# Optimization experiments

Hardware: AMD Instinct MI355X
Metric: run time of the kernel (lower is better)

Reference implementation:

```python
import jax, jax.numpy as jnp
import numpy as np


def setup_inputs() -> dict:
    key = jax.random.key(0)
    k1, k2 = jax.random.split(key)
    M, F, V = 4, 4, 6
    # positive messages / factor values (probabilities in real MPA), keep denominators safe
    IVF = jax.random.uniform(k1, (M, F, V), dtype=jnp.float32) + 0.1
    fa_n = jax.random.uniform(k2, (F, M, M, M), dtype=jnp.float32) + 0.1
    # canonical 4x6 SCMA factor graph: FN f connects to 3 VNs; each VN to 2 FNs
    FN_index = jnp.array([[0, 1, 2], [0, 3, 4], [1, 3, 5], [2, 4, 5]], dtype=jnp.int32)
    VN_index = jnp.array([[0, 0, 0, 1, 1, 2], [1, 2, 3, 2, 3, 3]], dtype=jnp.int32)
    w0 = jnp.ones((M, F, V), dtype=jnp.float32)  # nn.Parameter(torch.ones([4,4,6]))
    return {"num_M": 4, "num_FN": 4, "num_VN": 6, "IVF": IVF, "VN_index": VN_index,
            "m": 0, "n": 1, "FN_index": FN_index, "fa_n": fa_n, "w0": w0}


def _mpa_forward(IVF, fa_n, w0, FN_index, VN_index, num_M, num_FN, num_VN, m, n):
    M, F, V = num_M, num_FN, num_VN
    fidx = jnp.arange(F)
    # gather: g[k][mm, f] = IVF[mm, f, FN_index[f, k]]
    g0 = IVF[:, fidx, FN_index[:, 0]]  # [M, F]
    g1 = IVF[:, fidx, FN_index[:, 1]]
    g2 = IVF[:, fidx, FN_index[:, 2]]
    # FN -> VN messages: sum over the two other users' symbols (m2=b, m3=c)
    A0 = jnp.einsum('bf,cf,fcab->af', g1, g2, fa_n)  # to FN_index[:,0]
    A1 = jnp.einsum('bf,cf,fcba->af', g0, g2, fa_n)  # to FN_index[:,1]
    A2 = jnp.einsum('bf,cf,fabc->af', g0, g1, fa_n)  # to FN_index[:,2]
    IFV = jnp.zeros((M, F, V), IVF.dtype)
    IFV = IFV.at[:, fidx, FN_index[:, 0]].add(A0)
    IFV = IFV.at[:, fidx, FN_index[:, 1]].add(A1)
    IFV = IFV.at[:, fidx, FN_index[:, 2]].add(A2)
    if m >= n:  # static python ints -> plain branch, matches `if m < n`
        return IVF
    IVF_sum = IFV.mean(axis=0)  # [F, V]; == sum_i (1/M) IFV[i]
    vidx = jnp.arange(V)
    va, vb = VN_index[0], VN_index[1]  # the two FNs each VN connects to
    new_a = (1.0 / M) * IFV[:, vb, vidx] / IVF_sum[vb, vidx]  # [M, V]
    new_b = (1.0 / M) * IFV[:, va, vidx] / IVF_sum[va, vidx]
    IVF = IVF.at[:, va, vidx].set(new_a)
    IVF = IVF.at[:, vb, vidx].set(new_b)
    return IVF * w0


def reference(num_M, num_FN, num_VN, IVF, VN_index, m, n, FN_index, fa_n, w0):
    return _mpa_forward(IVF, fa_n, w0, FN_index, VN_index, num_M, num_FN, num_VN, m, n)
```

## Files before the change

### kernel.cpp

```cpp
#include <hip/hip_runtime.h>

__global__ __launch_bounds__(128) void mpa_kernel(
    const float* __restrict__ IVF,
    const int*   __restrict__ VN,
    const int*   __restrict__ mPtr,
    const int*   __restrict__ nPtr,
    const int*   __restrict__ FN,
    const float* __restrict__ fa,
    const float* __restrict__ w0,
    float*       __restrict__ out)
{
    __shared__ float sIVF[96];
    __shared__ float sIFV[96];
    __shared__ float sSum[24];

    const int t = threadIdx.x;

    if (t < 96) {
        sIVF[t] = IVF[t];
        sIFV[t] = 0.0f;
    }
    __syncthreads();

    if (t < 48) {
        const int kind = t >> 4;
        const int r    = t & 15;
        const int a    = r >> 2;
        const int f    = r & 3;
        const int j0 = FN[f * 3 + 0];
        const int j1 = FN[f * 3 + 1];
        const int j2 = FN[f * 3 + 2];

        const int jb = (kind == 0) ? j1 : j0;
        const int jc = (kind == 2) ? j1 : j2;

        float gb[4], gc[4];
        #pragma unroll
        for (int i = 0; i < 4; ++i) {
            gb[i] = sIVF[i * 24 + f * 6 + jb];
            gc[i] = sIVF[i * 24 + f * 6 + jc];
        }

        float acc = 0.0f;
        #pragma unroll
        for (int c = 0; c < 4; ++c) {
            #pragma unroll
            for (int b = 0; b < 4; ++b) {
                int faIdx;
                if (kind == 0)      faIdx = f * 64 + c * 16 + a * 4 + b;
                else if (kind == 1) faIdx = f * 64 + c * 16 + b * 4 + a;
                else                faIdx = f * 64 + a * 16 + b * 4 + c;
                acc += gb[b] * gc[c] * fa[faIdx];
            }
        }

        const int jout = (kind == 0) ? j0 : ((kind == 1) ? j1 : j2);
        sIFV[a * 24 + f * 6 + jout] = acc;
    }
    __syncthreads();

    if (t < 24) {
        sSum[t] = 0.25f * (sIFV[0 * 24 + t] + sIFV[1 * 24 + t] +
                           sIFV[2 * 24 + t] + sIFV[3 * 24 + t]);
    }
    __syncthreads();

    if (t < 96) {
        const int mv = mPtr[0];
        const int nv = nPtr[0];
        if (mv >= nv) {
            out[t] = sIVF == nullptr ? 0.0f : sIVF[t] * 0.0f + IVF[t];
        } else {
            const int a   = t / 24;
            const int rem = t - a * 24;
            const int f   = rem / 6;
            const int v   = rem - f * 6;
            const int va  = VN[v];
            const int vb  = VN[6 + v];
            float val;
            if (f == va)      val = 0.25f * sIFV[a * 24 + vb * 6 + v] / sSum[vb * 6 + v];
            else if (f == vb) val = 0.25f * sIFV[a * 24 + va * 6 + v] / sSum[va * 6 + v];
            else              val = sIVF[t];
            out[t] = val * w0[t];
        }
    }
}

extern "C" void kernel_launch(void* const* d_in, const int* in_sizes, int n_in,
                              void* d_out, int out_size, void* d_ws, size_t ws_size,
                              hipStream_t stream) {
    (void)in_sizes; (void)n_in; (void)d_ws; (void)ws_size; (void)out_size;
    const float* IVF = (const float*)d_in[3];
    const int*   VN  = (const int*)  d_in[4];
    const int*   m   = (const int*)  d_in[5];
    const int*   n   = (const int*)  d_in[6];
    const int*   FN  = (const int*)  d_in[7];
    const float* fa  = (const float*)d_in[8];
    const float* w0  = (const float*)d_in[9];
    float*       out = (float*)d_out;

    mpa_kernel<<<1, 128, 0, stream>>>(IVF, VN, m, n, FN, fa, w0, out);
}
```

Before: 9.621 us.

## Collapse MPA kernel into single wavefront using cross-lane bpermute instead of LDS barriers

Rewrites the kernel to run as one 64-lane wavefront with no shared memory or __syncthreads. Each lane issues all its global loads up front (IVF rows, fa slice, FN table, outputs' IVF/w0/VN) so their latencies overlap. The gathers are done with register selects, and the cross-lane sums and numerators come from ds_bpermute. Each lane produces two outputs. The cost is more redundant global loads per lane and more select instructions, in exchange for removing three barriers and the serialized load→compute→reduce phases.

```diff
diff --git a/kernel.cpp b/kernel.cpp
--- a/kernel.cpp
+++ b/kernel.cpp
@@ -1,6 +1,31 @@
 #include <hip/hip_runtime.h>
 
-__global__ __launch_bounds__(128) void mpa_kernel(
+
+__device__ __forceinline__ float sel6f(float r0, float r1, float r2, float r3,
+                                       float r4, float r5, int j) {
+    float x = r0;
+    x = (j == 1) ? r1 : x;
+    x = (j == 2) ? r2 : x;
+    x = (j == 3) ? r3 : x;
+    x = (j == 4) ? r4 : x;
+    x = (j == 5) ? r5 : x;
+    return x;
+}
+
+__device__ __forceinline__ int sel4i(int x0, int x1, int x2, int x3, int j) {
+    int x = x0;
+    x = (j == 1) ? x1 : x;
+    x = (j == 2) ? x2 : x;
+    x = (j == 3) ? x3 : x;
+    return x;
+}
+
+__device__ __forceinline__ float bperm(int lane, float v) {
+    return __int_as_float(
+        __builtin_amdgcn_ds_bpermute(lane << 2, __float_as_int(v)));
+}
+
+__global__ __launch_bounds__(64) void mpa_kernel(
     const float* __restrict__ IVF,
     const int*   __restrict__ VN,
     const int*   __restrict__ mPtr,
@@ -10,80 +35,107 @@
     const float* __restrict__ w0,
     float*       __restrict__ out)
 {
-    __shared__ float sIVF[96];
-    __shared__ float sIFV[96];
-    __shared__ float sSum[24];
+    const int l = threadIdx.x;
 
-    const int t = threadIdx.x;
+    const int kind = (l >= 32) ? 2 : (l >> 4);
+    const int a1   = (l >> 2) & 3;
+    const int f1   = l & 3;
 
-    if (t < 96) {
-        sIVF[t] = IVF[t];
-        sIFV[t] = 0.0f;
-    }
-    __syncthreads();
+    const int o1 = l;
+    const int o2 = 64 + (l & 31);
 
-    if (t < 48) {
-        const int kind = t >> 4;
-        const int r    = t & 15;
-        const int a    = r >> 2;
-        const int f    = r & 3;
-        const int j0 = FN[f * 3 + 0];
-        const int j1 = FN[f * 3 + 1];
-        const int j2 = FN[f * 3 + 2];
+    const int a2_1 = o1 / 24, rem1 = o1 - a2_1 * 24;
+    const int f2_1 = rem1 / 6, v2_1 = rem1 - f2_1 * 6;
+    const int a2_2 = o2 / 24, rem2 = o2 - a2_2 * 24;
+    const int f2_2 = rem2 / 6, v2_2 = rem2 - f2_2 * 6;
 
-        const int jb = (kind == 0) ? j1 : j0;
-        const int jc = (kind == 2) ? j1 : j2;
+    const int mv = mPtr[0];
+    const int nv = nPtr[0];
 
-        float gb[4], gc[4];
+    int fn[12];
+    #pragma unroll
+    for (int k = 0; k < 12; ++k) fn[k] = FN[k];
+
+    float row[4][6];
+    #pragma unroll
+    for (int i = 0; i < 4; ++i)
         #pragma unroll
-        for (int i = 0; i < 4; ++i) {
-            gb[i] = sIVF[i * 24 + f * 6 + jb];
-            gc[i] = sIVF[i * 24 + f * 6 + jc];
+        for (int j = 0; j < 6; ++j)
+            row[i][j] = IVF[i * 24 + f1 * 6 + j];
+
+    float fr[16];
+    #pragma unroll
+    for (int c = 0; c < 4; ++c)
+        #pragma unroll
+        for (int b = 0; b < 4; ++b) {
+            const int i0 = c * 16 + a1 * 4 + b;
+            const int i1 = c * 16 + b * 4 + a1;
+            const int i2 = a1 * 16 + b * 4 + c;
+            const int off = (kind == 0) ? i0 : ((kind == 1) ? i1 : i2);
+            fr[c * 4 + b] = fa[f1 * 64 + off];
         }
 
-        float acc = 0.0f;
+    const float iv1 = IVF[o1], wv1 = w0[o1];
+    const float iv2 = IVF[o2], wv2 = w0[o2];
+    const int va1 = VN[v2_1], vb1 = VN[6 + v2_1];
+    const int va2 = VN[v2_2], vb2 = VN[6 + v2_2];
+
+    const int j0 = sel4i(fn[0], fn[3], fn[6], fn[9],  f1);
+    const int j1 = sel4i(fn[1], fn[4], fn[7], fn[10], f1);
+    const int j2 = sel4i(fn[2], fn[5], fn[8], fn[11], f1);
+    const int jb = (kind == 0) ? j1 : j0;
+    const int jc = (kind == 2) ? j1 : j2;
+
+    float gb[4], gc[4];
+    #pragma unroll
+    for (int i = 0; i < 4; ++i) {
+        gb[i] = sel6f(row[i][0], row[i][1], row[i][2],
+                      row[i][3], row[i][4], row[i][5], jb);
+        gc[i] = sel6f(row[i][0], row[i][1], row[i][2],
+                      row[i][3], row[i][4], row[i][5], jc);
+    }
+
+    float acc = 0.0f;
+    #pragma unroll
+    for (int c = 0; c < 4; ++c)
         #pragma unroll
-        for (int c = 0; c < 4; ++c) {
-            #pragma unroll
-            for (int b = 0; b < 4; ++b) {
-                int faIdx;
-                if (kind == 0)      faIdx = f * 64 + c * 16 + a * 4 + b;
-                else if (kind == 1) faIdx = f * 64 + c * 16 + b * 4 + a;
-                else                faIdx = f * 64 + a * 16 + b * 4 + c;
-                acc += gb[b] * gc[c] * fa[faIdx];
-            }
-        }
+        for (int b = 0; b < 4; ++b)
+            acc += gb[b] * gc[c] * fr[c * 4 + b];
 
-        const int jout = (kind == 0) ? j0 : ((kind == 1) ? j1 : j2);
-        sIFV[a * 24 + f * 6 + jout] = acc;
+    float res[2];
+    const int  a2v[2] = {a2_1, a2_2};
+    const int  f2v[2] = {f2_1, f2_2};
+    const int  v2v[2] = {v2_1, v2_2};
+    const int  vav[2] = {va1, va2};
+    const int  vbv[2] = {vb1, vb2};
+    const float ivv[2] = {iv1, iv2};
+    const float wvv[2] = {wv1, wv2};
+
+    #pragma unroll
+    for (int q = 0; q < 2; ++q) {
+        const int f2 = f2v[q], v2 = v2v[q], a2 = a2v[q];
+        const int va = vav[q], vb = vbv[q];
+        const int fx = (f2 == va) ? vb : va;
+        const int fnA = sel4i(fn[0], fn[3], fn[6], fn[9],  fx);
+        const int fnB = sel4i(fn[1], fn[4], fn[7], fn[10], fx);
+        const int kx  = (fnA == v2) ? 0 : ((fnB == v2) ? 1 : 2);
+        const int base = kx * 16 + fx;
+        const float p0 = bperm(base + 0,  acc);
+        const float p1 = bperm(base + 4,  acc);
+        const float p2 = bperm(base + 8,  acc);
+        const float p3 = bperm(base + 12, acc);
+        const float sum = (p0 + p1) + (p2 + p3);
+        float num = p0;
+        num = (a2 == 1) ? p1 : num;
+        num = (a2 == 2) ? p2 : num;
+        num = (a2 == 3) ? p3 : num;
+        const bool incident = (f2 == va) || (f2 == vb);
+        const float val = incident ? (num / sum) : ivv[q];
+        res[q] = (mv >= nv) ? ivv[q] : val * wvv[q];
     }
-    __syncthreads();
 
-    if (t < 24) {
-        sSum[t] = 0.25f * (sIFV[0 * 24 + t] + sIFV[1 * 24 + t] +
-                           sIFV[2 * 24 + t] + sIFV[3 * 24 + t]);
-    }
-    __syncthreads();
-
-    if (t < 96) {
-        const int mv = mPtr[0];
-        const int nv = nPtr[0];
-        if (mv >= nv) {
-            out[t] = sIVF == nullptr ? 0.0f : sIVF[t] * 0.0f + IVF[t];
-        } else {
-            const int a   = t / 24;
-            const int rem = t - a * 24;
-            const int f   = rem / 6;
-            const int v   = rem - f * 6;
-            const int va  = VN[v];
-            const int vb  = VN[6 + v];
-            float val;
-            if (f == va)      val = 0.25f * sIFV[a * 24 + vb * 6 + v] / sSum[vb * 6 + v];
-            else if (f == vb) val = 0.25f * sIFV[a * 24 + va * 6 + v] / sSum[va * 6 + v];
-            else              val = sIVF[t];
-            out[t] = val * w0[t];
-        }
-    }
+    out[o1] = res[0];
+    if (l < 32) out[o2] = res[1];
 }
 
 extern "C" void kernel_launch(void* const* d_in, const int* in_sizes, int n_in,
@@ -99,5 +151,5 @@
     const float* w0  = (const float*)d_in[9];
     float*       out = (float*)d_out;
 
-    mpa_kernel<<<1, 128, 0, stream>>>(IVF, VN, m, n, FN, fa, w0, out);
+    mpa_kernel<<<1, 64, 0, stream>>>(IVF, VN, m, n, FN, fa, w0, out);
 }
```

Measured after the change: 9.724 us. No clear change (+1.1%).
